# Optimization experiments

Measured on AMD Instinct MI355X. Metric: run time of the kernel, lower is better.

## Reference

```python
import jax, jax.numpy as jnp
import numpy as np

N, IN, H0, H1 = 8192, 128, 512, 256
ITER = 10
EPS = 1e-5


def _bn(h, g, b):
    # BatchNorm1d in training mode: biased batch stats
    mu = h.mean(axis=0)
    var = h.var(axis=0)
    return g * (h - mu) * jax.lax.rsqrt(var + EPS) + b


def setup_inputs() -> dict:
    key = jax.random.key(0)
    ks = jax.random.split(key, 8)
    x = jax.random.normal(ks[0], (N, IN), dtype=jnp.float32)
    W = jax.random.uniform(ks[1], (N, N), dtype=jnp.float32)  # torch.rand
    W1 = jax.random.normal(ks[2], (H0, IN), dtype=jnp.float32) * (1.0 / np.sqrt(IN))
    b1 = jnp.zeros((H0,), jnp.float32)
    g1 = jnp.ones((H0,), jnp.float32)
    be1 = jnp.zeros((H0,), jnp.float32)
    W2 = jax.random.normal(ks[3], (H1, H0), dtype=jnp.float32) * (1.0 / np.sqrt(H0))
    b2 = jnp.zeros((H1,), jnp.float32)
    g2 = jnp.ones((H1,), jnp.float32)
    be2 = jnp.zeros((H1,), jnp.float32)
    fcw = jax.random.normal(ks[4], (1, H1), dtype=jnp.float32) * (1.0 / np.sqrt(H1))
    fcb = jnp.zeros((1,), jnp.float32)
    return {"x": x, "W": W, "W1": W1, "b1": b1, "g1": g1, "be1": be1,
            "W2": W2, "b2": b2, "g2": g2, "be2": be2, "fcw": fcw, "fcb": fcb}


def reference(x, W, W1, b1, g1, be1, W2, b2, g2, be2, fcw, fcb):
    h = jax.nn.leaky_relu(_bn(x @ W1.T + b1, g1, be1), 0.01)        # [N, H0]
    feats = jax.nn.leaky_relu(_bn(h @ W2.T + b2, g2, be2), 0.01)    # [N, H1]
    logits = feats @ fcw.T + fcb                                    # [N, 1]
    fn = jnp.linalg.norm(feats, axis=1, keepdims=True)              # [N, 1]
    pairwise_sim = (feats @ feats.T) / (fn @ fn.T)                  # [N, N]
    W_sym = (W + W.T) * 0.5
    PP = pairwise_sim * W_sym                                       # [N, N]
    unary = logits
    def body(i, lg):
        coef = 1.0 - 2.0 * jax.nn.sigmoid(lg)                       # (1-p) - p, [N,1]
        # E_i = sum_j (1-2 p_j) * PP[i, j]  -> matvec
        return unary + PP @ coef
    logits = jax.lax.fori_loop(0, ITER, body, logits)
    return logits
```

## Files before the change

kernel.cpp:

```cpp
#include <hip/hip_runtime.h>
#include <hip/hip_bf16.h>

#define NROWS 8192
#define NITER 10
#define ESCALE 1048576.0f
#define EINV   (1.0f / 1048576.0f)

typedef __attribute__((ext_vector_type(8))) short bf16x8;
typedef __attribute__((ext_vector_type(8))) unsigned short u16x8;
typedef __attribute__((ext_vector_type(16))) float f32x16;

__device__ __forceinline__ float bf2f(unsigned short u) {
  union { float f; unsigned int i; } c; c.i = ((unsigned int)u) << 16; return c.f;
}
__device__ __forceinline__ unsigned short f2bf(float f) {
  unsigned int x = __float_as_uint(f);
  unsigned int r = (x + 0x7FFFu + ((x >> 16) & 1u)) >> 16;
  return (unsigned short)r;
}

#define TRIS(b) ((b) * (257 - (b)) / 2)
__device__ __forceinline__ void tril_decode(int L, int& bi, int& bj) {
  int b = (int)((257.0f - sqrtf((float)(66049 - 8 * L))) * 0.5f);
  if (b > 127) b = 127;
  if (b < 0) b = 0;
  while (b < 127 && TRIS(b + 1) <= L) ++b;
  while (b > 0 && TRIS(b) > L) --b;
  bi = b;
  bj = b + (L - TRIS(b));
}

#define TRIS64(b) ((b) * (129 - (b)) / 2)
__device__ __forceinline__ void tril64_decode(int L, int& bi, int& bj) {
  int b = (int)((129.0f - sqrtf((float)(16641 - 8 * L))) * 0.5f);
  if (b > 63) b = 63;
  if (b < 0) b = 0;
  while (b < 63 && TRIS64(b + 1) <= L) ++b;
  while (b > 0 && TRIS64(b) > L) --b;
  bi = b;
  bj = b + (L - TRIS64(b));
}

__global__ __launch_bounds__(256) void cast3(const float* __restrict__ x,
                                             const float* __restrict__ W1,
                                             const float* __restrict__ W2,
                                             unsigned short* __restrict__ xb,
                                             unsigned short* __restrict__ w1b,
                                             unsigned short* __restrict__ w2b,
                                             unsigned long long* __restrict__ Z0) {
  int idx = blockIdx.x * 256 + threadIdx.x;
  if (idx < NROWS) Z0[idx] = 0ull;
  const float* src; unsigned short* dst; int l;
  if (idx < 131072) { src = x; dst = xb; l = idx; }
  else if (idx < 139264) { src = W1; dst = w1b; l = idx - 131072; }
  else if (idx < 155648) { src = W2; dst = w2b; l = idx - 139264; }
  else return;
  const float4* p = (const float4*)src + (size_t)l * 2;
  float4 a = p[0], b = p[1];
  u16x8 o;
  o[0] = f2bf(a.x); o[1] = f2bf(a.y); o[2] = f2bf(a.z); o[3] = f2bf(a.w);
  o[4] = f2bf(b.x); o[5] = f2bf(b.y); o[6] = f2bf(b.z); o[7] = f2bf(b.w);
  *(u16x8*)(dst + (size_t)l * 8) = o;
}

__global__ __launch_bounds__(256) void gemm_bt_mfma_stats(
    const unsigned short* __restrict__ A, const unsigned short* __restrict__ B,
    unsigned short* __restrict__ Cb, float* __restrict__ pS, float* __restrict__ pQ,
    int NN, int K) {
  __shared__ __align__(16) unsigned short Asw[4096];
  __shared__ __align__(16) unsigned short Bsw[4096];
  __shared__ float Sarr[4][64], Qarr[4][64];
  const int i0 = blockIdx.x * 64, j0 = blockIdx.y * 64;
  const int t = threadIdx.x;
  const int lane = t & 63;
  const int wv = t >> 6;
  const int wi = wv >> 1, wj = wv & 1;
  const int khalf = lane >> 5;

  f32x16 acc;
#pragma unroll
  for (int r = 0; r < 16; ++r) acc[r] = 0.f;

  const int lrow = t >> 2;
  const int lgp = (t & 3) * 2;
  const int arow = wi * 32 + (lane & 31);
  const int brow = wj * 32 + (lane & 31);
  const int nc = K >> 6;
#pragma unroll 1
  for (int c = 0; c < nc; ++c) {
    const unsigned short* sa = A + (size_t)(i0 + lrow) * K + c * 64 + lgp * 8;
    const unsigned short* sb = B + (size_t)(j0 + lrow) * K + c * 64 + lgp * 8;
    u16x8 va0 = *(const u16x8*)(sa);
    u16x8 va1 = *(const u16x8*)(sa + 8);
    u16x8 vb0 = *(const u16x8*)(sb);
    u16x8 vb1 = *(const u16x8*)(sb + 8);
    __syncthreads();
    int s0 = (lgp ^ (lrow & 7)) * 8;
    int s1 = ((lgp + 1) ^ (lrow & 7)) * 8;
    *(u16x8*)&Asw[lrow * 64 + s0] = va0;
    *(u16x8*)&Asw[lrow * 64 + s1] = va1;
    *(u16x8*)&Bsw[lrow * 64 + s0] = vb0;
    *(u16x8*)&Bsw[lrow * 64 + s1] = vb1;
    __syncthreads();
#pragma unroll
    for (int s = 0; s < 4; ++s) {
      int slot = s * 2 + khalf;
      bf16x8 a = *(const bf16x8*)&Asw[arow * 64 + ((slot ^ (arow & 7)) * 8)];
      bf16x8 b = *(const bf16x8*)&Bsw[brow * 64 + ((slot ^ (brow & 7)) * 8)];
      acc = __builtin_amdgcn_mfma_f32_32x32x16_bf16(a, b, acc, 0, 0, 0);
    }
  }
  float s = 0.f, q = 0.f;
#pragma unroll
  for (int r = 0; r < 16; ++r) {
    int rowl = (r & 3) + 8 * (r >> 2) + 4 * khalf;
    int coll = lane & 31;
    float v = acc[r];
    s += v; q += v * v;
    Cb[(size_t)(i0 + wi * 32 + rowl) * NN + j0 + wj * 32 + coll] = f2bf(v);
  }
  Sarr[wv][lane] = s;
  Qarr[wv][lane] = q;
  __syncthreads();
  if (t < 64) {
    int wjc = t >> 5, coll = t & 31;
    float st = (Sarr[wjc][coll] + Sarr[wjc][coll + 32]) +
               (Sarr[wjc + 2][coll] + Sarr[wjc + 2][coll + 32]);
    float qt = (Qarr[wjc][coll] + Qarr[wjc][coll + 32]) +
               (Qarr[wjc + 2][coll] + Qarr[wjc + 2][coll + 32]);
    pS[(size_t)blockIdx.x * NN + j0 + t] = st;
    pQ[(size_t)blockIdx.x * NN + j0 + t] = qt;
  }
}

__global__ void bn_finalize(const float* __restrict__ pS, const float* __restrict__ pQ,
                            const float* __restrict__ g, const float* __restrict__ be,
                            float2* __restrict__ ab, int C) {
  int c = blockIdx.x * 256 + threadIdx.x;
  if (c >= C) return;
  float s = 0.f, q = 0.f;
  for (int r = 0; r < 128; ++r) { s += pS[(size_t)r * C + c]; q += pQ[(size_t)r * C + c]; }
  const float invM = 1.f / 8192.f;
  float mu = s * invM;
  float var = q * invM - mu * mu;
  float rstd = rsqrtf(var + 1e-5f);
  float a = g[c] * rstd;
  ab[c] = make_float2(a, be[c] - mu * a);
}

__global__ __launch_bounds__(256) void bn_apply(const unsigned short* __restrict__ hraw,
                                                const float2* __restrict__ ab,
                                                unsigned short* __restrict__ hb,
                                                int Cmask) {
  size_t idx = (size_t)blockIdx.x * 256 + threadIdx.x;
  u16x8 v = *(const u16x8*)(hraw + idx * 8);
  int cb = (int)((idx * 8) & (size_t)Cmask);
  u16x8 o;
#pragma unroll
  for (int k = 0; k < 8; ++k) {
    float2 a = ab[cb + k];
    float r = a.x * bf2f(v[k]) + a.y;
    r = r >= 0.f ? r : 0.01f * r;
    o[k] = f2bf(r);
  }
  *(u16x8*)(hb + idx * 8) = o;
}

__global__ __launch_bounds__(256) void bn_rowfn(const unsigned short* __restrict__ fraw,
                                                const float2* __restrict__ ab,
                                                const float* __restrict__ fcw,
                                                const float* __restrict__ fcb,
                                                unsigned short* __restrict__ fnorm,
                                                float* __restrict__ unary,
                                                float* __restrict__ coef0) {
  const int lane = threadIdx.x & 63;
  const int row = blockIdx.x * 4 + (threadIdx.x >> 6);
  ushort4 v4 = *(const ushort4*)(fraw + (size_t)row * 256 + lane * 4);
  float4 w = *(const float4*)(fcw + lane * 4);
  int c = lane * 4;
  float2 a0 = ab[c], a1 = ab[c + 1], a2 = ab[c + 2], a3 = ab[c + 3];
  float f0 = a0.x * bf2f(v4.x) + a0.y; f0 = f0 >= 0.f ? f0 : 0.01f * f0;
  float f1 = a1.x * bf2f(v4.y) + a1.y; f1 = f1 >= 0.f ? f1 : 0.01f * f1;
  float f2 = a2.x * bf2f(v4.z) + a2.y; f2 = f2 >= 0.f ? f2 : 0.01f * f2;
  float f3 = a3.x * bf2f(v4.w) + a3.y; f3 = f3 >= 0.f ? f3 : 0.01f * f3;
  float ssq = f0 * f0 + f1 * f1 + f2 * f2 + f3 * f3;
  float dot = f0 * w.x + f1 * w.y + f2 * w.z + f3 * w.w;
#pragma unroll
  for (int o = 32; o; o >>= 1) { ssq += __shfl_xor(ssq, o); dot += __shfl_xor(dot, o); }
  float rfn = rsqrtf(ssq);
  *(ushort4*)(fnorm + (size_t)row * 256 + lane * 4) =
      make_ushort4(f2bf(f0 * rfn), f2bf(f1 * rfn), f2bf(f2 * rfn), f2bf(f3 * rfn));
  if (lane == 0) {
    float lg = dot + fcb[0];
    unary[row] = lg;
    coef0[row] = 1.f - 2.f / (1.f + __expf(-lg));
  }
}

__global__ __launch_bounds__(256) void ppbuild_sym(const unsigned short* __restrict__ fnorm,
                                                   const float* __restrict__ W,
                                                   unsigned short* __restrict__ PP) {
  int bi, bj;
  tril_decode(blockIdx.x, bi, bj);
  const int i0 = bi * 64, j0 = bj * 64;

  __shared__ __align__(16) unsigned char shm[18944];
  unsigned short* Asw = (unsigned short*)shm;
  unsigned short* Bsw = (unsigned short*)shm + 4736;
  float (*Wt)[68] = (float(*)[68])shm;
  unsigned short* OutD = (unsigned short*)shm;

  const int t = threadIdx.x;
  const int lane = t & 63;
  const int wv = t >> 6;
  const int wi = wv >> 1, wj = wv & 1;
  const int khalf = lane >> 5;

  const int jW = t >> 2, cbW = (t & 3) * 16;
  const float* srcT = W + (size_t)(j0 + jW) * NROWS + i0 + cbW;
  float4 wtv[4];
#pragma unroll
  for (int q = 0; q < 4; ++q) wtv[q] = *(const float4*)(srcT + q * 4);
  float wdv[16];
#pragma unroll
  for (int r = 0; r < 16; ++r) {
    int rowl = (r & 3) + 8 * (r >> 2) + 4 * khalf;
    wdv[r] = W[(size_t)(i0 + wi * 32 + rowl) * NROWS + (j0 + wj * 32 + (lane & 31))];
  }
  __builtin_amdgcn_sched_barrier(0);

  f32x16 acc;
#pragma unroll
  for (int r = 0; r < 16; ++r) acc[r] = 0.f;

  const int lrow = t >> 2;
  const int lgp = (t & 3) * 2;
  const int arow = wi * 32 + (lane & 31);
  const int brow = wj * 32 + (lane & 31);
#pragma unroll 1
  for (int c = 0; c < 4; ++c) {
    const unsigned short* sa = fnorm + (size_t)(i0 + lrow) * 256 + c * 64 + lgp * 8;
    const unsigned short* sb = fnorm + (size_t)(j0 + lrow) * 256 + c * 64 + lgp * 8;
    u16x8 va0 = *(const u16x8*)(sa);
    u16x8 va1 = *(const u16x8*)(sa + 8);
    u16x8 vb0 = *(const u16x8*)(sb);
    u16x8 vb1 = *(const u16x8*)(sb + 8);
    __syncthreads();
    int s0 = (lgp ^ (lrow & 7)) * 8;
    int s1 = ((lgp + 1) ^ (lrow & 7)) * 8;
    *(u16x8*)&Asw[lrow * 64 + s0] = va0;
    *(u16x8*)&Asw[lrow * 64 + s1] = va1;
    *(u16x8*)&Bsw[lrow * 64 + s0] = vb0;
    *(u16x8*)&Bsw[lrow * 64 + s1] = vb1;
    __syncthreads();
#pragma unroll
    for (int s = 0; s < 4; ++s) {
      int slot = s * 2 + khalf;
      bf16x8 a = *(const bf16x8*)&Asw[arow * 64 + ((slot ^ (arow & 7)) * 8)];
      bf16x8 b = *(const bf16x8*)&Bsw[brow * 64 + ((slot ^ (brow & 7)) * 8)];
      acc = __builtin_amdgcn_mfma_f32_32x32x16_bf16(a, b, acc, 0, 0, 0);
    }
  }

  __syncthreads();
  {
#pragma unroll
    for (int q = 0; q < 4; ++q) {
      Wt[jW][cbW + q * 4 + 0] = wtv[q].x; Wt[jW][cbW + q * 4 + 1] = wtv[q].y;
      Wt[jW][cbW + q * 4 + 2] = wtv[q].z; Wt[jW][cbW + q * 4 + 3] = wtv[q].w;
    }
  }
  __syncthreads();
  unsigned short pb[16];
#pragma unroll
  for (int r = 0; r < 16; ++r) {
    int rowl = (r & 3) + 8 * (r >> 2) + 4 * khalf;
    int coll = lane & 31;
    int il = wi * 32 + rowl, jl = wj * 32 + coll;
    float ws = 0.5f * (wdv[r] + Wt[jl][il]);
    pb[r] = f2bf(acc[r] * ws);
  }
  __syncthreads();
#pragma unroll
  for (int r = 0; r < 16; ++r) {
    int rowl = (r & 3) + 8 * (r >> 2) + 4 * khalf;
    int coll = lane & 31;
    OutD[(wi * 32 + rowl) * 74 + wj * 32 + coll] = pb[r];
  }
  __syncthreads();
  const int row = t >> 3;
  const int seg = t & 7;
#pragma unroll
  for (int q = 0; q < 2; ++q) {
    int rr = row + q * 32;
    const unsigned int* pd = (const unsigned int*)(OutD + rr * 74 + seg * 8);
    union { u16x8 v; unsigned int u[4]; } dd;
#pragma unroll
    for (int k = 0; k < 4; ++k) dd.u[k] = pd[k];
    *(u16x8*)(PP + (size_t)(i0 + rr) * NROWS + j0 + seg * 8) = dd.v;
  }
}

__global__ __launch_bounds__(256) void ppmv_atomic(
    const unsigned short* __restrict__ PP,
    const float* __restrict__ unary,
    const long long* __restrict__ Zprev,
    const float* __restrict__ coef0,
    unsigned long long* __restrict__ Zacc,
    unsigned long long* __restrict__ Zzero) {
  int bi, bj;
  tril64_decode(blockIdx.x, bi, bj);
  const int i0 = bi * 128, j0 = bj * 128;
  const int t = threadIdx.x;

  __shared__ __align__(16) unsigned short tile[128][132];
  __shared__ float cj[128], ci[128];
  __shared__ float Tw[8][128];

  const int r = t >> 1, h = (t & 1) * 64;
  u16x8 tv[8];
  {
    const unsigned short* src = PP + (size_t)(i0 + r) * NROWS + j0 + h;
#pragma unroll
    for (int q = 0; q < 8; ++q) tv[q] = *(const u16x8*)(src + q * 8);
  }
  if (bi == bj && Zzero != nullptr && t < 128) Zzero[i0 + t] = 0ull;
  {
    int myrow = (t < 128) ? (j0 + t) : (i0 + (t - 128));
    float c;
    if (Zprev) {
      float lg = unary[myrow] + (float)Zprev[myrow] * EINV;
      c = 1.f - 2.f / (1.f + __expf(-lg));
    } else {
      c = coef0[myrow];
    }
    if (t < 128) cj[t] = c;
    else ci[t - 128] = c;
  }
#pragma unroll
  for (int q = 0; q < 8; ++q) *(u16x8*)&tile[r][h + q * 8] = tv[q];
  __syncthreads();
  {
    float a = 0.f;
#pragma unroll
    for (int q = 0; q < 8; ++q) {
      u16x8 v = tv[q];
      float4 c0 = *(const float4*)&cj[h + q * 8];
      float4 c1 = *(const float4*)&cj[h + q * 8 + 4];
      a += bf2f(v[0]) * c0.x + bf2f(v[1]) * c0.y + bf2f(v[2]) * c0.z + bf2f(v[3]) * c0.w;
      a += bf2f(v[4]) * c1.x + bf2f(v[5]) * c1.y + bf2f(v[6]) * c1.z + bf2f(v[7]) * c1.w;
    }
    a += __shfl_xor(a, 1);
    if ((t & 1) == 0)
      atomicAdd(&Zacc[i0 + r], (unsigned long long)(long long)llrintf(a * ESCALE));
  }
  {
    const int c4 = (t & 31) * 4, rg = t >> 5;
    float a0 = 0.f, a1 = 0.f, a2 = 0.f, a3 = 0.f;
#pragma unroll
    for (int k = 0; k < 16; ++k) {
      int row = rg * 16 + k;
      ushort4 v = *(const ushort4*)&tile[row][c4];
      float s = ci[row];
      a0 += bf2f(v.x) * s; a1 += bf2f(v.y) * s;
      a2 += bf2f(v.z) * s; a3 += bf2f(v.w) * s;
    }
    Tw[rg][c4] = a0; Tw[rg][c4 + 1] = a1;
    Tw[rg][c4 + 2] = a2; Tw[rg][c4 + 3] = a3;
  }
  __syncthreads();
  if (t < 128 && bi != bj) {
    float s = ((Tw[0][t] + Tw[1][t]) + (Tw[2][t] + Tw[3][t])) +
              ((Tw[4][t] + Tw[5][t]) + (Tw[6][t] + Tw[7][t]));
    atomicAdd(&Zacc[j0 + t], (unsigned long long)(long long)llrintf(s * ESCALE));
  }
}

__global__ __launch_bounds__(256) void final_out(const long long* __restrict__ Z,
                                                 const float* __restrict__ unary,
                                                 float* __restrict__ out) {
  int row = blockIdx.x * 256 + threadIdx.x;
  out[row] = unary[row] + (float)Z[row] * EINV;
}

extern "C" void kernel_launch(void* const* d_in, const int* in_sizes, int n_in,
                              void* d_out, int out_size, void* d_ws, size_t ws_size,
                              hipStream_t stream) {
  const float* x   = (const float*)d_in[0];
  const float* W   = (const float*)d_in[1];
  const float* W1  = (const float*)d_in[2];
  const float* g1  = (const float*)d_in[4];
  const float* be1 = (const float*)d_in[5];
  const float* W2  = (const float*)d_in[6];
  const float* g2  = (const float*)d_in[8];
  const float* be2 = (const float*)d_in[9];
  const float* fcw = (const float*)d_in[10];
  const float* fcb = (const float*)d_in[11];
  float* out = (float*)d_out;

  char* ws = (char*)d_ws;
  unsigned short* hraw = (unsigned short*)(ws + 0);
  unsigned short* fraw = (unsigned short*)(ws + 8388608);
  float* pS1   = (float*)(ws + 12582912);
  float* pQ1   = (float*)(ws + 12845056);
  float* pS2   = (float*)(ws + 13107200);
  float* pQ2   = (float*)(ws + 13238272);
  float2* ab1  = (float2*)(ws + 13369344);
  float2* ab2  = (float2*)(ws + 13373440);
  unsigned short* fnorm = (unsigned short*)(ws + 13375488);
  float* unary = (float*)(ws + 17569792);
  float* coefA = (float*)(ws + 17602560);
  unsigned short* hb  = (unsigned short*)(ws + 17668096);
  unsigned short* xb  = (unsigned short*)(ws + 26056704);
  unsigned short* w1b = (unsigned short*)(ws + 28153856);
  unsigned short* w2b = (unsigned short*)(ws + 28284928);
  unsigned short* PP  = (unsigned short*)(ws + 28547072);
  unsigned long long* Z0 = (unsigned long long*)(ws + 162764800);
  unsigned long long* Z1 = (unsigned long long*)(ws + 162830336);
  unsigned long long* Z2 = (unsigned long long*)(ws + 162895872);
  if (ws_size < (size_t)162961408) return;
  unsigned long long* Z[3] = {Z0, Z1, Z2};

  cast3<<<608, 256, 0, stream>>>(x, W1, W2, xb, w1b, w2b, Z0);
  gemm_bt_mfma_stats<<<dim3(128, 8), 256, 0, stream>>>(xb, w1b, hraw, pS1, pQ1, 512, 128);
  bn_finalize<<<2, 256, 0, stream>>>(pS1, pQ1, g1, be1, ab1, 512);
  bn_apply<<<2048, 256, 0, stream>>>(hraw, ab1, hb, 511);
  gemm_bt_mfma_stats<<<dim3(128, 4), 256, 0, stream>>>(hb, w2b, fraw, pS2, pQ2, 256, 512);
  bn_finalize<<<1, 256, 0, stream>>>(pS2, pQ2, g2, be2, ab2, 256);
  bn_rowfn<<<2048, 256, 0, stream>>>(fraw, ab2, fcw, fcb, fnorm, unary, coefA);
  ppbuild_sym<<<8256, 256, 0, stream>>>(fnorm, W, PP);
  for (int it = 1; it <= NITER; ++it) {
    const long long* zp = (it == 1) ? nullptr : (const long long*)Z[(it + 1) % 3];
    unsigned long long* za = Z[(it - 1) % 3];
    unsigned long long* zz = (it < NITER) ? Z[it % 3] : nullptr;
    ppmv_atomic<<<2080, 256, 0, stream>>>(PP, unary, zp, coefA, za, zz);
  }
  final_out<<<32, 256, 0, stream>>>((const long long*)Z[(NITER - 1) % 3], unary, out);
}
```

Measured before the change: 285.7 us.

## Fuse BN1 apply into second GEMM prologue and stage W tiles in LDS

Removes the separate bn_apply kernel by applying the layer-1 batchnorm scale/shift and leaky ReLU to A tiles as they are loaded in the second GEMM, using per-channel coefficients cached in shared memory. This saves one full read/write pass over the 8192x512 hidden activations and one launch. The PP build kernel now stages both the W tile and its transposed tile in LDS up front, where before it held one in registers with scattered per-element loads. Its LDS footprint grows from about 19 KB to 50 KB, which may lower occupancy on a kernel launched with 8256 blocks.

```diff
diff --git a/kernel.cpp b/kernel.cpp
--- a/kernel.cpp
+++ b/kernel.cpp
@@ -65,17 +65,24 @@
 
 __global__ __launch_bounds__(256) void gemm_bt_mfma_stats(
     const unsigned short* __restrict__ A, const unsigned short* __restrict__ B,
+    const float2* __restrict__ abA,
     unsigned short* __restrict__ Cb, float* __restrict__ pS, float* __restrict__ pQ,
     int NN, int K) {
   __shared__ __align__(16) unsigned short Asw[4096];
   __shared__ __align__(16) unsigned short Bsw[4096];
   __shared__ float Sarr[4][64], Qarr[4][64];
+  __shared__ float2 abLds[512];
   const int i0 = blockIdx.x * 64, j0 = blockIdx.y * 64;
   const int t = threadIdx.x;
   const int lane = t & 63;
   const int wv = t >> 6;
   const int wi = wv >> 1, wj = wv & 1;
   const int khalf = lane >> 5;
+
+  if (abA) {
+    abLds[t] = abA[t];
+    if (t + 256 < K) abLds[t + 256] = abA[t + 256];
+  }
 
   f32x16 acc;
 #pragma unroll
@@ -95,6 +102,20 @@
     u16x8 vb0 = *(const u16x8*)(sb);
     u16x8 vb1 = *(const u16x8*)(sb + 8);
     __syncthreads();
+    if (abA) {
+      int cb0 = c * 64 + lgp * 8;
+#pragma unroll
+      for (int k = 0; k < 8; ++k) {
+        float2 a0 = abLds[cb0 + k];
+        float2 a1 = abLds[cb0 + 8 + k];
+        float r0 = a0.x * bf2f((unsigned short)va0[k]) + a0.y;
+        float r1 = a1.x * bf2f((unsigned short)va1[k]) + a1.y;
+        r0 = r0 >= 0.f ? r0 : 0.01f * r0;
+        r1 = r1 >= 0.f ? r1 : 0.01f * r1;
+        va0[k] = (unsigned short)f2bf(r0);
+        va1[k] = (unsigned short)f2bf(r1);
+      }
+    }
     int s0 = (lgp ^ (lrow & 7)) * 8;
     int s1 = ((lgp + 1) ^ (lrow & 7)) * 8;
     *(u16x8*)&Asw[lrow * 64 + s0] = va0;
@@ -146,24 +167,6 @@
   float rstd = rsqrtf(var + 1e-5f);
   float a = g[c] * rstd;
   ab[c] = make_float2(a, be[c] - mu * a);
-}
-
-__global__ __launch_bounds__(256) void bn_apply(const unsigned short* __restrict__ hraw,
-                                                const float2* __restrict__ ab,
-                                                unsigned short* __restrict__ hb,
-                                                int Cmask) {
-  size_t idx = (size_t)blockIdx.x * 256 + threadIdx.x;
-  u16x8 v = *(const u16x8*)(hraw + idx * 8);
-  int cb = (int)((idx * 8) & (size_t)Cmask);
-  u16x8 o;
-#pragma unroll
-  for (int k = 0; k < 8; ++k) {
-    float2 a = ab[cb + k];
-    float r = a.x * bf2f(v[k]) + a.y;
-    r = r >= 0.f ? r : 0.01f * r;
-    o[k] = f2bf(r);
-  }
-  *(u16x8*)(hb + idx * 8) = o;
 }
 
 __global__ __launch_bounds__(256) void bn_rowfn(const unsigned short* __restrict__ fraw,
@@ -204,11 +207,12 @@
   tril_decode(blockIdx.x, bi, bj);
   const int i0 = bi * 64, j0 = bj * 64;
 
-  __shared__ __align__(16) unsigned char shm[18944];
+  __shared__ __align__(16) unsigned char shm[51200];
   unsigned short* Asw = (unsigned short*)shm;
-  unsigned short* Bsw = (unsigned short*)shm + 4736;
-  float (*Wt)[68] = (float(*)[68])shm;
+  unsigned short* Bsw = (unsigned short*)(shm + 8192);
   unsigned short* OutD = (unsigned short*)shm;
+  float (*Wt)[68] = (float(*)[68])(shm + 16384);
+  float (*Wd)[68] = (float(*)[68])(shm + 33792);
 
   const int t = threadIdx.x;
   const int lane = t & 63;
@@ -216,18 +220,20 @@
   const int wi = wv >> 1, wj = wv & 1;
   const int khalf = lane >> 5;
 
-  const int jW = t >> 2, cbW = (t & 3) * 16;
-  const float* srcT = W + (size_t)(j0 + jW) * NROWS + i0 + cbW;
-  float4 wtv[4];
-#pragma unroll
-  for (int q = 0; q < 4; ++q) wtv[q] = *(const float4*)(srcT + q * 4);
-  float wdv[16];
-#pragma unroll
-  for (int r = 0; r < 16; ++r) {
-    int rowl = (r & 3) + 8 * (r >> 2) + 4 * khalf;
-    wdv[r] = W[(size_t)(i0 + wi * 32 + rowl) * NROWS + (j0 + wj * 32 + (lane & 31))];
-  }
-  __builtin_amdgcn_sched_barrier(0);
+  {
+    const int jW = t >> 2, cbW = (t & 3) * 16;
+    const float* srcT = W + (size_t)(j0 + jW) * NROWS + i0 + cbW;
+    const float* srcD = W + (size_t)(i0 + jW) * NROWS + j0 + cbW;
+#pragma unroll
+    for (int q = 0; q < 4; ++q) {
+      float4 vT = *(const float4*)(srcT + q * 4);
+      float4 vD = *(const float4*)(srcD + q * 4);
+      Wt[jW][cbW + q * 4 + 0] = vT.x; Wt[jW][cbW + q * 4 + 1] = vT.y;
+      Wt[jW][cbW + q * 4 + 2] = vT.z; Wt[jW][cbW + q * 4 + 3] = vT.w;
+      Wd[jW][cbW + q * 4 + 0] = vD.x; Wd[jW][cbW + q * 4 + 1] = vD.y;
+      Wd[jW][cbW + q * 4 + 2] = vD.z; Wd[jW][cbW + q * 4 + 3] = vD.w;
+    }
+  }
 
   f32x16 acc;
 #pragma unroll
@@ -263,24 +269,15 @@
   }
 
   __syncthreads();
-  {
-#pragma unroll
-    for (int q = 0; q < 4; ++q) {
-      Wt[jW][cbW + q * 4 + 0] = wtv[q].x; Wt[jW][cbW + q * 4 + 1] = wtv[q].y;
-      Wt[jW][cbW + q * 4 + 2] = wtv[q].z; Wt[jW][cbW + q * 4 + 3] = wtv[q].w;
-    }
-  }
-  __syncthreads();
   unsigned short pb[16];
 #pragma unroll
   for (int r = 0; r < 16; ++r) {
     int rowl = (r & 3) + 8 * (r >> 2) + 4 * khalf;
     int coll = lane & 31;
     int il = wi * 32 + rowl, jl = wj * 32 + coll;
-    float ws = 0.5f * (wdv[r] + Wt[jl][il]);
+    float ws = 0.5f * (Wd[il][jl] + Wt[jl][il]);
     pb[r] = f2bf(acc[r] * ws);
   }
-  __syncthreads();
 #pragma unroll
   for (int r = 0; r < 16; ++r) {
     int rowl = (r & 3) + 8 * (r >> 2) + 4 * khalf;
@@ -410,7 +407,6 @@
   unsigned short* fnorm = (unsigned short*)(ws + 13375488);
   float* unary = (float*)(ws + 17569792);
   float* coefA = (float*)(ws + 17602560);
-  unsigned short* hb  = (unsigned short*)(ws + 17668096);
   unsigned short* xb  = (unsigned short*)(ws + 26056704);
   unsigned short* w1b = (unsigned short*)(ws + 28153856);
   unsigned short* w2b = (unsigned short*)(ws + 28284928);
@@ -422,10 +418,11 @@
   unsigned long long* Z[3] = {Z0, Z1, Z2};
 
   cast3<<<608, 256, 0, stream>>>(x, W1, W2, xb, w1b, w2b, Z0);
-  gemm_bt_mfma_stats<<<dim3(128, 8), 256, 0, stream>>>(xb, w1b, hraw, pS1, pQ1, 512, 128);
+  gemm_bt_mfma_stats<<<dim3(128, 8), 256, 0, stream>>>(xb, w1b, nullptr, hraw,
+                                                       pS1, pQ1, 512, 128);
   bn_finalize<<<2, 256, 0, stream>>>(pS1, pQ1, g1, be1, ab1, 512);
-  bn_apply<<<2048, 256, 0, stream>>>(hraw, ab1, hb, 511);
-  gemm_bt_mfma_stats<<<dim3(128, 4), 256, 0, stream>>>(hb, w2b, fraw, pS2, pQ2, 256, 512);
+  gemm_bt_mfma_stats<<<dim3(128, 4), 256, 0, stream>>>(hraw, w2b, ab1, fraw,
+                                                       pS2, pQ2, 256, 512);
   bn_finalize<<<1, 256, 0, stream>>>(pS2, pQ2, g2, be2, ab2, 256);
   bn_rowfn<<<2048, 256, 0, stream>>>(fraw, ab2, fcw, fcb, fnorm, unary, coefA);
   ppbuild_sym<<<8256, 256, 0, stream>>>(fnorm, W, PP);
```

New measurement: 299.2 us. 1.05x slower.
